# Kernel optimization log

Hardware: AMD Instinct MI355X
Metric: run time of the kernel (lower is better)

Reference implementation:

```python
import jax, jax.numpy as jnp
import numpy as np

N = 50000      # nodes
DEG = 16       # avg degree
E = N * DEG    # edges
F_IN = 256
F_OUT = 128
ALPHA = 0.2    # leaky-relu slope


def setup_inputs() -> dict:
    key = jax.random.key(0)
    k1, k2, k3, k4, k5, k6 = jax.random.split(key, 6)
    x = jax.random.normal(k1, (N, F_IN), dtype=jnp.float32)
    # edges sorted by source (required by the module's `m` construction)
    src = jnp.repeat(jnp.arange(N, dtype=jnp.int32), DEG)
    dst = jax.random.randint(k2, (E,), 0, N, dtype=jnp.int32)
    edge = jnp.stack([src, dst])  # (2, E)
    s_w = 1.414 * np.sqrt(2.0 / (F_IN + F_OUT))   # xavier_normal gain=1.414
    s_a = 1.414 * np.sqrt(2.0 / (1 + 2 * F_OUT))
    W_high = jax.random.normal(k3, (F_IN, F_OUT), jnp.float32) * s_w
    W_low = jax.random.normal(k4, (F_IN, F_OUT), jnp.float32) * s_w
    a_high = jax.random.normal(k5, (1, 2 * F_OUT), jnp.float32) * s_a
    a_low = jax.random.normal(k6, (1, 2 * F_OUT), jnp.float32) * s_a
    return {"x": x, "edge": edge, "W_high": W_high, "W_low": W_low,
            "a_high": a_high, "a_low": a_low}


def _leaky(v):
    return jnp.where(v >= 0, v, ALPHA * v)


def _elu6(v):
    return jnp.minimum(jnp.where(v > 0, v, jnp.expm1(v)), 6.0)


def reference(x, edge, W_high, W_low, a_high, a_low):
    src, dst = edge[0], edge[1]
    n = x.shape[0]
    h_hi = x @ W_high            # (N, F_OUT)
    h_lo = x @ W_low

    # per-edge attention logits: a . [h[src], h[dst]]
    a_hi_s, a_hi_d = a_high[0, :F_OUT], a_high[0, F_OUT:]
    a_lo_s, a_lo_d = a_low[0, :F_OUT], a_low[0, F_OUT:]
    logit_hi = (h_hi @ a_hi_s)[src] + (h_hi @ a_hi_d)[dst]   # (E,)
    logit_lo = (h_lo @ a_lo_s)[src] + (h_lo @ a_lo_d)[dst]
    e_hi = jnp.exp(-_leaky(logit_hi))
    e_lo = jnp.exp(-_leaky(logit_lo))

    # sparse rowsum: spmm(edge, e, [N,N], ones) == segment_sum over src
    rowsum_hi = jax.ops.segment_sum(e_hi, src, num_segments=n)[:, None]
    rowsum_lo = jax.ops.segment_sum(e_lo, src, num_segments=n)[:, None]

    # relu6 (dropout p=0 / eval mode -> identity)
    e_hi = jnp.clip(e_hi, 0.0, 6.0)
    e_lo = jnp.clip(e_lo, 0.0, 6.0)

    # per-edge features, then m @ (.) == segment-sum of edge features by source
    he_hi = h_hi[src] + h_hi[dst]                # (E, F_OUT)
    he_lo = h_lo[src] - h_lo[dst]
    hn_hi = jax.ops.segment_sum(he_hi, src, num_segments=n)  # (N, F_OUT)
    hn_lo = jax.ops.segment_sum(he_lo, src, num_segments=n)

    # spmm(edge, e, [N,N], hn): row i sums e_ij * hn[j] over its edges
    hp_hi = jax.ops.segment_sum(e_hi[:, None] * hn_hi[dst], src, num_segments=n)
    hp_lo = jax.ops.segment_sum(e_lo[:, None] * hn_lo[dst], src, num_segments=n)

    hp_hi = hp_hi / (rowsum_hi + 1e-16)
    hp_lo = hp_lo / (rowsum_lo + 1e-16)
    h_prime = 0.5 * (hp_hi + hp_lo)
    return _elu6(h_prime)  # concat=True branch
```

## Files before the change

kernel.cpp:

```cpp
#include <hip/hip_runtime.h>
#include <hip/hip_bf16.h>
#include <math.h>

#define NN    50000
#define DEG   16
#define FIN   256
#define FOUT  128
#define EE    (NN * DEG)
#define ALPHA 0.2f

#define BM 64
#define BN 256

#define SLW 32

typedef __hip_bfloat16 bf16;
typedef _Float16 f16;
typedef __attribute__((ext_vector_type(8))) _Float16 f16x8;
typedef __attribute__((ext_vector_type(8))) short short8;
typedef __attribute__((ext_vector_type(4))) float f32x4;
typedef __attribute__((ext_vector_type(8))) unsigned short u16x8;
typedef __attribute__((ext_vector_type(8))) unsigned int u32x8;

__global__ __launch_bounds__(256) void split_w_kernel(
    const float* __restrict__ Wh, const float* __restrict__ Wl,
    bf16* __restrict__ Wcat2)
{
    const int k = blockIdx.x;
    const int n = threadIdx.x;
    const float w = (n < FOUT) ? Wh[(size_t)k * FOUT + n]
                               : Wl[(size_t)k * FOUT + (n - FOUT)];
    const bf16 hi = __float2bfloat16(w);
    const bf16 lo = __float2bfloat16(w - __bfloat162float(hi));
    Wcat2[(size_t)n * 512 + k]       = hi;
    Wcat2[(size_t)n * 512 + 256 + k] = lo;
}

__global__ __launch_bounds__(256) void gemm_mfma_kernel(
    const float* __restrict__ x, const bf16* __restrict__ Wcat2,
    const float* __restrict__ a_high, const float* __restrict__ a_low,
    f16* __restrict__ h16, float* __restrict__ sd_s, float* __restrict__ sd_d)
{
    __shared__ bf16 Ah[2][BM * 32];
    __shared__ bf16 Al[2][BM * 32];

    const int t    = threadIdx.x;
    const int lane = t & 63;
    const int w    = t >> 6;
    const int r0   = blockIdx.x * BM;

    f32x4 acc[4][4] = {};

    const int arow = t >> 2;
    const float* xsrc = x + (size_t)min(r0 + arow, NN - 1) * FIN + (t & 3) * 8;
    const int awaddr = arow * 64 + ((((t & 3)) + (arow >> 1)) & 3) * 16;

    const int lr = lane & 15, lg = lane >> 4;

    const bf16* bbase = Wcat2 + ((size_t)(w * 64 + lr) * 512) + lg * 8;

    short8 xh[8], xl[8];
#pragma unroll
    for (int s = 0; s < 8; ++s) {
        const float4 xa = *(const float4*)(xsrc + s * 32 + 0);
        const float4 xb = *(const float4*)(xsrc + s * 32 + 4);
        const float f[8] = {xa.x, xa.y, xa.z, xa.w, xb.x, xb.y, xb.z, xb.w};
#pragma unroll
        for (int j = 0; j < 8; ++j) {
            const bf16 h = __float2bfloat16(f[j]);
            const bf16 l = __float2bfloat16(f[j] - __bfloat162float(h));
            ((bf16*)&xh[s])[j] = h;
            ((bf16*)&xl[s])[j] = l;
        }
    }

    *(short8*)((char*)Ah[0] + awaddr) = xh[0];
    *(short8*)((char*)Al[0] + awaddr) = xl[0];
    __syncthreads();

#pragma unroll
    for (int s = 0; s < 8; ++s) {
        const int cur = s & 1, nxt = cur ^ 1;

        if (s < 7) {
            *(short8*)((char*)Ah[nxt] + awaddr) = xh[s + 1];
            *(short8*)((char*)Al[nxt] + awaddr) = xl[s + 1];
        }

        short8 wa[4], wb[4];
#pragma unroll
        for (int ni = 0; ni < 4; ++ni)
            wa[ni] = *(const short8*)(bbase + (size_t)ni * 16 * 512 + s * 32);
#pragma unroll
        for (int ni = 0; ni < 4; ++ni)
            wb[ni] = *(const short8*)(bbase + (size_t)ni * 16 * 512 + s * 32 + 256);

        short8 fh[4], fl[4];
#pragma unroll
        for (int mi = 0; mi < 4; ++mi) {
            const int row  = mi * 16 + lr;
            const int slot = (lg + (row >> 1)) & 3;
            fh[mi] = *(const short8*)((const char*)Ah[cur] + row * 64 + slot * 16);
        }
#pragma unroll
        for (int mi = 0; mi < 4; ++mi)
#pragma unroll
            for (int ni = 0; ni < 4; ++ni)
                acc[mi][ni] = __builtin_amdgcn_mfma_f32_16x16x32_bf16(
                    fh[mi], wa[ni], acc[mi][ni], 0, 0, 0);
#pragma unroll
        for (int mi = 0; mi < 4; ++mi)
#pragma unroll
            for (int ni = 0; ni < 4; ++ni)
                acc[mi][ni] = __builtin_amdgcn_mfma_f32_16x16x32_bf16(
                    fh[mi], wb[ni], acc[mi][ni], 0, 0, 0);
#pragma unroll
        for (int mi = 0; mi < 4; ++mi) {
            const int row  = mi * 16 + lr;
            const int slot = (lg + (row >> 1)) & 3;
            fl[mi] = *(const short8*)((const char*)Al[cur] + row * 64 + slot * 16);
        }
#pragma unroll
        for (int mi = 0; mi < 4; ++mi)
#pragma unroll
            for (int ni = 0; ni < 4; ++ni)
                acc[mi][ni] = __builtin_amdgcn_mfma_f32_16x16x32_bf16(
                    fl[mi], wa[ni], acc[mi][ni], 0, 0, 0);

        __syncthreads();
    }

    const int slc_base = (w < 2) ? w * 4 : (w - 2) * 4;
    const int off      = ((w < 2) ? 0 : 16) + lr;
#pragma unroll
    for (int mi = 0; mi < 4; ++mi) {
        const int rowb = r0 + mi * 16 + lg * 4;
#pragma unroll
        for (int r = 0; r < 4; ++r) {
            const int row = rowb + r;
            if (row >= NN) continue;
#pragma unroll
            for (int ni = 0; ni < 4; ++ni)
                h16[((size_t)(slc_base + ni) * NN + row) * SLW + off] =
                    (f16)acc[mi][ni][r];
        }
    }

    __syncthreads();

    const float* aa = (w < 2) ? a_high : a_low;
    const int cb = (w < 2) ? w * 64 : (w - 2) * 64;
    float as_[4], ad_[4];
#pragma unroll
    for (int ni = 0; ni < 4; ++ni) {
        as_[ni] = aa[cb + ni * 16 + lr];
        ad_[ni] = aa[FOUT + cb + ni * 16 + lr];
    }
    float* sred = (float*)Ah[0];
#pragma unroll
    for (int mi = 0; mi < 4; ++mi)
#pragma unroll
        for (int r = 0; r < 4; ++r) {
            float ps = 0.f, pd = 0.f;
#pragma unroll
            for (int ni = 0; ni < 4; ++ni) {
                ps += acc[mi][ni][r] * as_[ni];
                pd += acc[mi][ni][r] * ad_[ni];
            }
#pragma unroll
            for (int o = 1; o < 16; o <<= 1) {
                ps += __shfl_xor(ps, o);
                pd += __shfl_xor(pd, o);
            }
            if (lr == 0) {
                const int row = mi * 16 + lg * 4 + r;
                sred[(w * 2 + 0) * 64 + row] = ps;
                sred[(w * 2 + 1) * 64 + row] = pd;
            }
        }
    __syncthreads();
    if (t < 64) {
        const int row = r0 + t;
        if (row < NN) {
            const float s_hi = sred[0 * 64 + t] + sred[2 * 64 + t];
            const float d_hi = sred[1 * 64 + t] + sred[3 * 64 + t];
            const float s_lo = sred[4 * 64 + t] + sred[6 * 64 + t];
            const float d_lo = sred[5 * 64 + t] + sred[7 * 64 + t];
            ((float2*)sd_s)[row] = make_float2(s_hi, s_lo);
            ((float2*)sd_d)[row] = make_float2(d_hi, d_lo);
        }
    }
}

__global__ __launch_bounds__(256) void weight_kernel(
    const int* __restrict__ dst, const float* __restrict__ sd_s,
    const float* __restrict__ sd_d, unsigned short* __restrict__ d16,
    unsigned int* __restrict__ w32)
{
    const int wid  = (blockIdx.x * 256 + threadIdx.x) >> 6;
    const int lane = threadIdx.x & 63;
    if (wid >= NN) return;

    const int e    = lane & 15;
    const int d_my = dst[wid * DEG + e];
    const bool whi = (lane & 16) == 0;
    const float2 s2 = ((const float2*)sd_s)[wid];
    const float2 dd = ((const float2*)sd_d)[d_my];
    const float l   = whi ? (s2.x + dd.x) : (s2.y + dd.y);
    const float ev  = __expf(-(l >= 0.f ? l : ALPHA * l));

    float rs = ev;
    rs += __shfl_xor(rs, 1);
    rs += __shfl_xor(rs, 2);
    rs += __shfl_xor(rs, 4);
    rs += __shfl_xor(rs, 8);
    const float wn = fminf(ev, 6.f) / (rs + 1e-16f);
    const float wl = __shfl(wn, e + 16);

    if (lane < 16) {
        const f16 wh16 = (f16)wn, wl16 = (f16)wl;
        const unsigned a = *(const unsigned short*)&wh16;
        const unsigned b = *(const unsigned short*)&wl16;
        d16[wid * DEG + e] = (unsigned short)d_my;
        w32[wid * DEG + e] = a | (b << 16);
    }
}

__global__ __launch_bounds__(320) void hn_slice_kernel(
    const f16* __restrict__ h16, const unsigned short* __restrict__ d16,
    f16* __restrict__ hn16)
{
    const int sl    = blockIdx.x & 7;
    const int chunk = blockIdx.x >> 3;
    const int wv    = threadIdx.x >> 6;
    const int lane  = threadIdx.x & 63;
    const int k     = lane >> 3;
    const int c     = (lane >> 1) & 3;
    const int hf    = lane & 1;
    const int n     = (chunk * 5 + wv) * 8 + k;

    const char* hsl = (const char*)(h16 + (size_t)sl * NN * SLW);
    const float sgn = (c < 2) ? 1.f : -1.f;
    const unsigned coff = (unsigned)c * 16u;
    const unsigned noff = (unsigned)n * 64u + coff;

    const u16x8 d8 = *(const u16x8*)(d16 + n * DEG + hf * 8);
    const f16x8 own = *(const f16x8*)(hsl + noff);

    float acc[8] = {};
#pragma unroll
    for (int t = 0; t < 8; ++t) {
        const unsigned d = (unsigned)d8[t];
        const f16x8 g = *(const f16x8*)(hsl + (d * 64u + coff));
#pragma unroll
        for (int j = 0; j < 8; ++j) acc[j] = fmaf(sgn, (float)g[j], acc[j]);
    }
#pragma unroll
    for (int j = 0; j < 8; ++j) acc[j] += __shfl_xor(acc[j], 1);

    if (hf == 0) {
        f16x8 o;
#pragma unroll
        for (int j = 0; j < 8; ++j) o[j] = (f16)fmaf((float)own[j], 16.f, acc[j]);
        *(f16x8*)((char*)(hn16 + (size_t)sl * NN * SLW) + noff) = o;
    }
}

__global__ __launch_bounds__(320) void out_slice_kernel(
    const f16* __restrict__ hn16, const unsigned short* __restrict__ d16,
    const unsigned int* __restrict__ w32, float* __restrict__ out)
{
    const int sl    = blockIdx.x & 7;
    const int chunk = blockIdx.x >> 3;
    const int wv    = threadIdx.x >> 6;
    const int lane  = threadIdx.x & 63;
    const int k     = lane >> 3;
    const int c     = (lane >> 1) & 3;
    const int hf    = lane & 1;
    const int n     = (chunk * 5 + wv) * 8 + k;
    const bool chi  = (c < 2);

    const char* hsl = (const char*)(hn16 + (size_t)sl * NN * SLW);
    const unsigned coff = (unsigned)c * 16u;

    const u16x8 d8 = *(const u16x8*)(d16 + n * DEG + hf * 8);
    const u32x8 w8 = *(const u32x8*)(w32 + n * DEG + hf * 8);

    float acc[8] = {};
#pragma unroll
    for (int t = 0; t < 8; ++t) {
        const unsigned wp = w8[t];
        const unsigned short wu = chi ? (unsigned short)(wp & 0xffffu)
                                      : (unsigned short)(wp >> 16);
        const float w = (float)(*(const f16*)&wu);
        const f16x8 g = *(const f16x8*)(hsl + ((unsigned)d8[t] * 64u + coff));
#pragma unroll
        for (int j = 0; j < 8; ++j) acc[j] = fmaf(w, (float)g[j], acc[j]);
    }
#pragma unroll
    for (int j = 0; j < 8; ++j) acc[j] += __shfl_xor(acc[j], 1);

    float4 v0, v1;
#pragma unroll
    for (int j = 0; j < 8; ++j) {
        const float p = __shfl_xor(acc[j], 4);
        float v = 0.5f * (acc[j] + p);
        v = (v > 0.f) ? v : (__expf(v) - 1.f);
        v = fminf(v, 6.f);
        if (j < 4) ((float*)&v0)[j] = v; else ((float*)&v1)[j - 4] = v;
    }
    if (chi && hf == 0) {
        float* op = out + (size_t)n * FOUT + sl * 16 + c * 8;
        *(float4*)op       = v0;
        *(float4*)(op + 4) = v1;
    }
}

extern "C" void kernel_launch(void* const* d_in, const int* in_sizes, int n_in,
                              void* d_out, int out_size, void* d_ws, size_t ws_size,
                              hipStream_t stream)
{
    const float* x      = (const float*)d_in[0];
    const int*   edge   = (const int*)d_in[1];
    const float* Wh     = (const float*)d_in[2];
    const float* Wl     = (const float*)d_in[3];
    const float* a_high = (const float*)d_in[4];
    const float* a_low  = (const float*)d_in[5];
    const int*   dstv   = edge + EE;

    char* ws = (char*)d_ws;
    f16*   h16   = (f16*)ws;
    f16*   hn16  = (f16*)(ws + 25600000);
    bf16*  Wcat2 = (bf16*)(ws + 51200000);
    float* sd_s  = (float*)(ws + 51800000);
    float* sd_d  = (float*)(ws + 52200000);
    unsigned short* d16 = (unsigned short*)(ws + 52600000);
    unsigned int*   w32 = (unsigned int*)(ws + 54400000);

    split_w_kernel<<<dim3(256), dim3(256), 0, stream>>>(Wh, Wl, Wcat2);
    gemm_mfma_kernel<<<dim3((NN + BM - 1) / BM), dim3(256), 0, stream>>>(
        x, Wcat2, a_high, a_low, h16, sd_s, sd_d);
    weight_kernel<<<dim3((NN + 3) / 4), dim3(256), 0, stream>>>(dstv, sd_s, sd_d, d16, w32);
    hn_slice_kernel<<<dim3(8 * 1250), dim3(320), 0, stream>>>(h16, d16, hn16);
    out_slice_kernel<<<dim3(8 * 1250), dim3(320), 0, stream>>>(hn16, d16, w32, (float*)d_out);
}
```

Before: 142.5 us.

## Stage W tiles through LDS with async global_load_lds double buffering

The GEMM kernel used to read the split bf16 weight matrix straight from global memory into registers at every K step. It now copies 32-column weight tiles into double-buffered LDS with global_load_lds, issued two steps ahead, and waits on them with explicit vmcnt/lgkmcnt counters and s_barrier. The aim is to hide weight-load latency behind MFMA work and to stop each block from re-reading weights uncoalesced. In exchange it uses much more LDS (about 64KB more per block), which can lower occupancy, and it relies on hand-counted waitcnt values.

```diff
diff --git a/kernel.cpp b/kernel.cpp
--- a/kernel.cpp
+++ b/kernel.cpp
@@ -43,6 +43,8 @@
 {
     __shared__ bf16 Ah[2][BM * 32];
     __shared__ bf16 Al[2][BM * 32];
+    __shared__ bf16 Ba[2][BN * 32];
+    __shared__ bf16 Bb[2][BN * 32];
 
     const int t    = threadIdx.x;
     const int lane = t & 63;
@@ -55,9 +57,15 @@
     const float* xsrc = x + (size_t)min(r0 + arow, NN - 1) * FIN + (t & 3) * 8;
     const int awaddr = arow * 64 + ((((t & 3)) + (arow >> 1)) & 3) * 16;
 
+    int bro[4], bsl[4];
+#pragma unroll
+    for (int i = 0; i < 4; ++i) {
+        const int idx = t + i * 256;
+        bro[i] = idx >> 2;
+        bsl[i] = ((idx & 3) - (bro[i] >> 1)) & 3;
+    }
+
     const int lr = lane & 15, lg = lane >> 4;
-
-    const bf16* bbase = Wcat2 + ((size_t)(w * 64 + lr) * 512) + lg * 8;
 
     short8 xh[8], xl[8];
 #pragma unroll
@@ -73,35 +81,70 @@
             ((bf16*)&xl[s])[j] = l;
         }
     }
-
-    *(short8*)((char*)Ah[0] + awaddr) = xh[0];
-    *(short8*)((char*)Al[0] + awaddr) = xl[0];
-    __syncthreads();
+#pragma unroll
+    for (int b = 0; b < 2; ++b) {
+        const int c0 = b * 32;
+#pragma unroll
+        for (int i = 0; i < 4; ++i) {
+            __builtin_amdgcn_global_load_lds(
+                (const __attribute__((address_space(1))) void*)
+                    (Wcat2 + (size_t)bro[i] * 512 + c0 + bsl[i] * 8),
+                (__attribute__((address_space(3))) void*)((char*)Ba[b] + (t + i * 256) * 16),
+                16, 0, 0);
+            __builtin_amdgcn_global_load_lds(
+                (const __attribute__((address_space(1))) void*)
+                    (Wcat2 + (size_t)bro[i] * 512 + 256 + c0 + bsl[i] * 8),
+                (__attribute__((address_space(3))) void*)((char*)Bb[b] + (t + i * 256) * 16),
+                16, 0, 0);
+        }
+        *(short8*)((char*)Ah[b] + awaddr) = xh[b];
+        *(short8*)((char*)Al[b] + awaddr) = xl[b];
+    }
+    asm volatile("s_waitcnt vmcnt(8) lgkmcnt(0)" ::: "memory");
+    __builtin_amdgcn_s_barrier();
 
 #pragma unroll
     for (int s = 0; s < 8; ++s) {
-        const int cur = s & 1, nxt = cur ^ 1;
-
-        if (s < 7) {
-            *(short8*)((char*)Ah[nxt] + awaddr) = xh[s + 1];
-            *(short8*)((char*)Al[nxt] + awaddr) = xl[s + 1];
-        }
-
-        short8 wa[4], wb[4];
-#pragma unroll
-        for (int ni = 0; ni < 4; ++ni)
-            wa[ni] = *(const short8*)(bbase + (size_t)ni * 16 * 512 + s * 32);
-#pragma unroll
-        for (int ni = 0; ni < 4; ++ni)
-            wb[ni] = *(const short8*)(bbase + (size_t)ni * 16 * 512 + s * 32 + 256);
-
-        short8 fh[4], fl[4];
+        const int cur = s & 1;
+
+        short8 fh[4], fl[4], wa[4], wb[4];
 #pragma unroll
         for (int mi = 0; mi < 4; ++mi) {
             const int row  = mi * 16 + lr;
             const int slot = (lg + (row >> 1)) & 3;
             fh[mi] = *(const short8*)((const char*)Ah[cur] + row * 64 + slot * 16);
-        }
+            fl[mi] = *(const short8*)((const char*)Al[cur] + row * 64 + slot * 16);
+        }
+#pragma unroll
+        for (int ni = 0; ni < 4; ++ni) {
+            const int row  = w * 64 + ni * 16 + lr;
+            const int slot = (lg + (row >> 1)) & 3;
+            wa[ni] = *(const short8*)((const char*)Ba[cur] + row * 64 + slot * 16);
+            wb[ni] = *(const short8*)((const char*)Bb[cur] + row * 64 + slot * 16);
+        }
+        asm volatile("s_waitcnt lgkmcnt(0)" ::: "memory");
+        __builtin_amdgcn_sched_barrier(0);
+        __builtin_amdgcn_s_barrier();
+
+        if (s < 6) {
+            const int c2 = (s + 2) * 32;
+#pragma unroll
+            for (int i = 0; i < 4; ++i) {
+                __builtin_amdgcn_global_load_lds(
+                    (const __attribute__((address_space(1))) void*)
+                        (Wcat2 + (size_t)bro[i] * 512 + c2 + bsl[i] * 8),
+                    (__attribute__((address_space(3))) void*)((char*)Ba[cur] + (t + i * 256) * 16),
+                    16, 0, 0);
+                __builtin_amdgcn_global_load_lds(
+                    (const __attribute__((address_space(1))) void*)
+                        (Wcat2 + (size_t)bro[i] * 512 + 256 + c2 + bsl[i] * 8),
+                    (__attribute__((address_space(3))) void*)((char*)Bb[cur] + (t + i * 256) * 16),
+                    16, 0, 0);
+            }
+            *(short8*)((char*)Ah[cur] + awaddr) = xh[s + 2];
+            *(short8*)((char*)Al[cur] + awaddr) = xl[s + 2];
+        }
+
 #pragma unroll
         for (int mi = 0; mi < 4; ++mi)
 #pragma unroll
@@ -115,19 +158,19 @@
                 acc[mi][ni] = __builtin_amdgcn_mfma_f32_16x16x32_bf16(
                     fh[mi], wb[ni], acc[mi][ni], 0, 0, 0);
 #pragma unroll
-        for (int mi = 0; mi < 4; ++mi) {
-            const int row  = mi * 16 + lr;
-            const int slot = (lg + (row >> 1)) & 3;
-            fl[mi] = *(const short8*)((const char*)Al[cur] + row * 64 + slot * 16);
-        }
-#pragma unroll
         for (int mi = 0; mi < 4; ++mi)
 #pragma unroll
             for (int ni = 0; ni < 4; ++ni)
                 acc[mi][ni] = __builtin_amdgcn_mfma_f32_16x16x32_bf16(
                     fl[mi], wa[ni], acc[mi][ni], 0, 0, 0);
 
-        __syncthreads();
+        if (s < 6) {
+            asm volatile("s_waitcnt vmcnt(8) lgkmcnt(0)" ::: "memory");
+            __builtin_amdgcn_s_barrier();
+        } else if (s == 6) {
+            asm volatile("s_waitcnt vmcnt(0) lgkmcnt(0)" ::: "memory");
+            __builtin_amdgcn_s_barrier();
+        }
     }
 
     const int slc_base = (w < 2) ? w * 4 : (w - 2) * 4;
```

After: 132.2 us. -7.3%, faster.

## Load x fragments directly from global into MFMA registers, dropping LDS staging

Applied to the files above, without the earlier changes.

The GEMM kernel no longer splits x into bf16 hi/lo parts and stages them in double-buffered LDS. Each wave now loads its own A fragments straight from global memory and converts them in registers, using a bit-mask truncation for the hi part. This removes the LDS traffic and the per-step barriers, and launch bounds now request 2 blocks per CU. In exchange, each of the four waves re-reads the same x rows from global/L2 (4x redundant loads), and the truncation changes rounding of the hi part slightly.

```diff
diff --git a/kernel.cpp b/kernel.cpp
--- a/kernel.cpp
+++ b/kernel.cpp
@@ -36,72 +36,52 @@
     Wcat2[(size_t)n * 512 + 256 + k] = lo;
 }
 
-__global__ __launch_bounds__(256) void gemm_mfma_kernel(
+__global__ __launch_bounds__(256, 2) void gemm_mfma_kernel(
     const float* __restrict__ x, const bf16* __restrict__ Wcat2,
     const float* __restrict__ a_high, const float* __restrict__ a_low,
     f16* __restrict__ h16, float* __restrict__ sd_s, float* __restrict__ sd_d)
 {
-    __shared__ bf16 Ah[2][BM * 32];
-    __shared__ bf16 Al[2][BM * 32];
+    __shared__ float sred[8 * 64];
 
     const int t    = threadIdx.x;
     const int lane = t & 63;
     const int w    = t >> 6;
     const int r0   = blockIdx.x * BM;
+    const int lr   = lane & 15, lg = lane >> 4;
 
     f32x4 acc[4][4] = {};
 
-    const int arow = t >> 2;
-    const float* xsrc = x + (size_t)min(r0 + arow, NN - 1) * FIN + (t & 3) * 8;
-    const int awaddr = arow * 64 + ((((t & 3)) + (arow >> 1)) & 3) * 16;
-
-    const int lr = lane & 15, lg = lane >> 4;
-
-    const bf16* bbase = Wcat2 + ((size_t)(w * 64 + lr) * 512) + lg * 8;
-
-    short8 xh[8], xl[8];
+    const float* aptr[4];
+#pragma unroll
+    for (int mi = 0; mi < 4; ++mi)
+        aptr[mi] = x + (size_t)min(r0 + mi * 16 + lr, NN - 1) * FIN + lg * 8;
+
+    const bf16* bbase = Wcat2 + (size_t)(w * 64 + lr) * 512 + lg * 8;
+
 #pragma unroll
     for (int s = 0; s < 8; ++s) {
-        const float4 xa = *(const float4*)(xsrc + s * 32 + 0);
-        const float4 xb = *(const float4*)(xsrc + s * 32 + 4);
-        const float f[8] = {xa.x, xa.y, xa.z, xa.w, xb.x, xb.y, xb.z, xb.w};
-#pragma unroll
-        for (int j = 0; j < 8; ++j) {
-            const bf16 h = __float2bfloat16(f[j]);
-            const bf16 l = __float2bfloat16(f[j] - __bfloat162float(h));
-            ((bf16*)&xh[s])[j] = h;
-            ((bf16*)&xl[s])[j] = l;
-        }
-    }
-
-    *(short8*)((char*)Ah[0] + awaddr) = xh[0];
-    *(short8*)((char*)Al[0] + awaddr) = xl[0];
-    __syncthreads();
-
-#pragma unroll
-    for (int s = 0; s < 8; ++s) {
-        const int cur = s & 1, nxt = cur ^ 1;
-
-        if (s < 7) {
-            *(short8*)((char*)Ah[nxt] + awaddr) = xh[s + 1];
-            *(short8*)((char*)Al[nxt] + awaddr) = xl[s + 1];
-        }
-
-        short8 wa[4], wb[4];
-#pragma unroll
-        for (int ni = 0; ni < 4; ++ni)
+        short8 fh[4], fl[4], wa[4], wb[4];
+
+#pragma unroll
+        for (int mi = 0; mi < 4; ++mi) {
+            const float4 xa = *(const float4*)(aptr[mi] + s * 32);
+            const float4 xb = *(const float4*)(aptr[mi] + s * 32 + 4);
+            const float f[8] = {xa.x, xa.y, xa.z, xa.w, xb.x, xb.y, xb.z, xb.w};
+#pragma unroll
+            for (int j = 0; j < 8; ++j) {
+                const unsigned b = __float_as_uint(f[j]);
+                ((unsigned short*)&fh[mi])[j] = (unsigned short)(b >> 16);
+                const float hi_f = __uint_as_float(b & 0xFFFF0000u);
+                ((bf16*)&fl[mi])[j] = __float2bfloat16(f[j] - hi_f);
+            }
+        }
+
+#pragma unroll
+        for (int ni = 0; ni < 4; ++ni) {
             wa[ni] = *(const short8*)(bbase + (size_t)ni * 16 * 512 + s * 32);
-#pragma unroll
-        for (int ni = 0; ni < 4; ++ni)
             wb[ni] = *(const short8*)(bbase + (size_t)ni * 16 * 512 + s * 32 + 256);
-
-        short8 fh[4], fl[4];
-#pragma unroll
-        for (int mi = 0; mi < 4; ++mi) {
-            const int row  = mi * 16 + lr;
-            const int slot = (lg + (row >> 1)) & 3;
-            fh[mi] = *(const short8*)((const char*)Ah[cur] + row * 64 + slot * 16);
-        }
+        }
+
 #pragma unroll
         for (int mi = 0; mi < 4; ++mi)
 #pragma unroll
@@ -115,19 +95,11 @@
                 acc[mi][ni] = __builtin_amdgcn_mfma_f32_16x16x32_bf16(
                     fh[mi], wb[ni], acc[mi][ni], 0, 0, 0);
 #pragma unroll
-        for (int mi = 0; mi < 4; ++mi) {
-            const int row  = mi * 16 + lr;
-            const int slot = (lg + (row >> 1)) & 3;
-            fl[mi] = *(const short8*)((const char*)Al[cur] + row * 64 + slot * 16);
-        }
-#pragma unroll
         for (int mi = 0; mi < 4; ++mi)
 #pragma unroll
             for (int ni = 0; ni < 4; ++ni)
                 acc[mi][ni] = __builtin_amdgcn_mfma_f32_16x16x32_bf16(
                     fl[mi], wa[ni], acc[mi][ni], 0, 0, 0);
-
-        __syncthreads();
     }
 
     const int slc_base = (w < 2) ? w * 4 : (w - 2) * 4;
@@ -146,8 +118,6 @@
         }
     }
 
-    __syncthreads();
-
     const float* aa = (w < 2) ? a_high : a_low;
     const int cb = (w < 2) ? w * 64 : (w - 2) * 64;
     float as_[4], ad_[4];
@@ -156,7 +126,6 @@
         as_[ni] = aa[cb + ni * 16 + lr];
         ad_[ni] = aa[FOUT + cb + ni * 16 + lr];
     }
-    float* sred = (float*)Ah[0];
 #pragma unroll
     for (int mi = 0; mi < 4; ++mi)
 #pragma unroll
```

After: 164.4 us. +15.4%, slower.
